# Optimization experiments

Hardware: AMD Instinct MI355X
Metric: run time of the kernel (lower is better)

Reference implementation:

```python
import jax, jax.numpy as jnp
import numpy as np

IN_FEATURES = 4096
OUT_FEATURES = 11008
BATCH = 16


def setup_inputs() -> dict:
    key = jax.random.key(0)
    k_x, k_w, k_s, k_b = jax.random.split(key, 4)
    x = jax.random.normal(k_x, (BATCH, IN_FEATURES), dtype=jnp.float32)
    # symmetric int8 weights stored as int32 for jax portability (values in [-127, 127])
    weight_int8 = jax.random.randint(k_w, (OUT_FEATURES, IN_FEATURES), -127, 128, dtype=jnp.int32)
    # per-output-channel scales, small positive values typical of int8 quantization
    weight_scale = jax.random.uniform(k_s, (OUT_FEATURES,), dtype=jnp.float32, minval=0.005, maxval=0.02)
    bias = jax.random.normal(k_b, (OUT_FEATURES,), dtype=jnp.float32)
    return {"x": x, "weight_int8": weight_int8, "weight_scale": weight_scale, "bias": bias}


def reference(x, weight_int8, weight_scale, bias):
    # Dequantize: w_dq[o, i] = int8[o, i] * scale[o]  -> fp32 [OUT, IN]
    w_dq = weight_int8.astype(x.dtype) * weight_scale[:, None]
    # F.linear: y = x @ w_dq.T + bias  -> [BATCH, OUT]
    return jnp.einsum("bi,oi->bo", x, w_dq) + bias
```

## Files before the change

kernel.cpp:

```cpp
#include <hip/hip_runtime.h>

#define IN_F   4096
#define OUT_F  11008
#define BATCH  16
#define TK     512
#define CO     16
#define BLOCK  256
#define SPLITK 4
#define KCHUNK (IN_F / SPLITK)

typedef int   i32x4 __attribute__((ext_vector_type(4)));

__global__ __launch_bounds__(BLOCK) void init_out_kernel(
    const float* __restrict__ bias, float* __restrict__ out)
{
    int idx = blockIdx.x * BLOCK + threadIdx.x;
    if (idx < BATCH * OUT_F) {
        int o = idx % OUT_F;
        out[idx] = bias[o];
    }
}

__global__ __launch_bounds__(BLOCK) void qlin_kernel(
    const float* __restrict__ x,
    const int*   __restrict__ w,
    const float* __restrict__ scale,
    float* __restrict__ out)
{
    __shared__ float xs[BATCH][TK];

    const int tid = threadIdx.x;
    const int tx  = tid & 63;
    const int ty  = tid >> 6;
    const int o0  = blockIdx.x * CO + ty * 4;
    const int kb  = blockIdx.y * KCHUNK;

    const i32x4* __restrict__ wbase = (const i32x4*)(w + (size_t)o0 * IN_F);

    float acc[64];
    #pragma unroll
    for (int i = 0; i < 64; ++i) acc[i] = 0.f;

    for (int k0 = kb; k0 < kb + KCHUNK; k0 += TK) {
        #pragma unroll
        for (int j = 0; j < (BATCH * TK / 4) / BLOCK; ++j) {
            int f  = tid + j * BLOCK;
            int b  = f >> 7;
            int kc = f & 127;
            const float* src = x + (size_t)b * IN_F + k0 + kc * 4;
            void* dst = (char*)&xs[0][0] + (size_t)f * 16;
            __builtin_amdgcn_global_load_lds(
                (const __attribute__((address_space(1))) void*)src,
                (__attribute__((address_space(3))) void*)dst,
                16, 0, 0);
        }
        __syncthreads();

        #pragma unroll
        for (int it = 0; it < TK / 256; ++it) {
            const int    kl  = it * 256 + tx * 4;
            const size_t kg4 = (size_t)((k0 >> 2) + it * 64 + tx);

            i32x4 w0 = __builtin_nontemporal_load(wbase + kg4);
            i32x4 w1 = __builtin_nontemporal_load(wbase + kg4 + 1 * (IN_F / 4));
            i32x4 w2 = __builtin_nontemporal_load(wbase + kg4 + 2 * (IN_F / 4));
            i32x4 w3 = __builtin_nontemporal_load(wbase + kg4 + 3 * (IN_F / 4));

            float wf[4][4];
            #pragma unroll
            for (int e = 0; e < 4; ++e) {
                wf[0][e] = (float)w0[e];
                wf[1][e] = (float)w1[e];
                wf[2][e] = (float)w2[e];
                wf[3][e] = (float)w3[e];
            }

            #pragma unroll
            for (int bc = 0; bc < 4; ++bc) {
                float4 xv[4];
                #pragma unroll
                for (int bb = 0; bb < 4; ++bb)
                    xv[bb] = *(const float4*)&xs[bc * 4 + bb][kl];

                #pragma unroll
                for (int r = 0; r < 4; ++r)
                    #pragma unroll
                    for (int bb = 0; bb < 4; ++bb) {
                        float a = acc[r * 16 + bc * 4 + bb];
                        a += wf[r][0] * xv[bb].x;
                        a += wf[r][1] * xv[bb].y;
                        a += wf[r][2] * xv[bb].z;
                        a += wf[r][3] * xv[bb].w;
                        acc[r * 16 + bc * 4 + bb] = a;
                    }
            }
        }
        __syncthreads();
    }

    #pragma unroll
    for (int wd = 32; wd >= 1; wd >>= 1) {
        const bool upper = (tx & wd) != 0;
        #pragma unroll
        for (int i = 0; i < wd; ++i) {
            float lo = acc[i]      + __shfl_xor(acc[i],      wd);
            float hi = acc[i + wd] + __shfl_xor(acc[i + wd], wd);
            acc[i] = upper ? hi : lo;
        }
    }

    const int o = o0 + (tx >> 4);
    const int b = tx & 15;
    atomicAdd(&out[(size_t)b * OUT_F + o], acc[0] * scale[o]);
}

extern "C" void kernel_launch(void* const* d_in, const int* in_sizes, int n_in,
                              void* d_out, int out_size, void* d_ws, size_t ws_size,
                              hipStream_t stream) {
    const float* x     = (const float*)d_in[0];
    const int*   w     = (const int*)d_in[1];
    const float* scale = (const float*)d_in[2];
    const float* bias  = (const float*)d_in[3];
    float* out = (float*)d_out;

    init_out_kernel<<<(BATCH * OUT_F + BLOCK - 1) / BLOCK, BLOCK, 0, stream>>>(bias, out);

    dim3 grid(OUT_F / CO, SPLITK);
    qlin_kernel<<<grid, dim3(BLOCK), 0, stream>>>(x, w, scale, out);
}
```

Measured before the change: 259.4 us.

## Stage full K chunk in LDS and prefetch all weight loads upfront

Replaces the tiled K loop with a single load of the block's entire K chunk of activations into shared memory. All weight vectors for the chunk are issued up front into registers before computing. This is meant to increase memory-level parallelism and remove intermediate barriers. In exchange it doubles LDS usage and raises register pressure, which can reduce occupancy.

```diff
diff --git a/kernel.cpp b/kernel.cpp
--- a/kernel.cpp
+++ b/kernel.cpp
@@ -3,11 +3,11 @@
 #define IN_F   4096
 #define OUT_F  11008
 #define BATCH  16
-#define TK     512
 #define CO     16
 #define BLOCK  256
 #define SPLITK 4
 #define KCHUNK (IN_F / SPLITK)
+#define NIT    (KCHUNK / 256)
 
 typedef int   i32x4 __attribute__((ext_vector_type(4)));
 
@@ -27,7 +27,7 @@
     const float* __restrict__ scale,
     float* __restrict__ out)
 {
-    __shared__ float xs[BATCH][TK];
+    __shared__ float xs[BATCH][KCHUNK];
 
     const int tid = threadIdx.x;
     const int tx  = tid & 63;
@@ -41,61 +41,59 @@
     #pragma unroll
     for (int i = 0; i < 64; ++i) acc[i] = 0.f;
 
-    for (int k0 = kb; k0 < kb + KCHUNK; k0 += TK) {
+    #pragma unroll
+    for (int j = 0; j < (BATCH * KCHUNK / 4) / BLOCK; ++j) {
+        int f  = tid + j * BLOCK;
+        int b  = f >> 8;
+        int kc = f & 255;
+        const float* src = x + (size_t)b * IN_F + kb + kc * 4;
+        void* dst = (char*)&xs[0][0] + (size_t)f * 16;
+        __builtin_amdgcn_global_load_lds(
+            (const __attribute__((address_space(1))) void*)src,
+            (__attribute__((address_space(3))) void*)dst,
+            16, 0, 0);
+    }
+    __syncthreads();
+
+    i32x4 wr[NIT][4];
+    #pragma unroll
+    for (int it = 0; it < NIT; ++it) {
+        const size_t kg4 = (size_t)((kb >> 2) + it * 64 + tx);
         #pragma unroll
-        for (int j = 0; j < (BATCH * TK / 4) / BLOCK; ++j) {
-            int f  = tid + j * BLOCK;
-            int b  = f >> 7;
-            int kc = f & 127;
-            const float* src = x + (size_t)b * IN_F + k0 + kc * 4;
-            void* dst = (char*)&xs[0][0] + (size_t)f * 16;
-            __builtin_amdgcn_global_load_lds(
-                (const __attribute__((address_space(1))) void*)src,
-                (__attribute__((address_space(3))) void*)dst,
-                16, 0, 0);
-        }
-        __syncthreads();
+        for (int r = 0; r < 4; ++r)
+            wr[it][r] = __builtin_nontemporal_load(wbase + kg4 + (size_t)r * (IN_F / 4));
+    }
+
+    #pragma unroll
+    for (int it = 0; it < NIT; ++it) {
+        const int kl = it * 256 + tx * 4;
+
+        float wf[4][4];
+        #pragma unroll
+        for (int r = 0; r < 4; ++r)
+            #pragma unroll
+            for (int e = 0; e < 4; ++e)
+                wf[r][e] = (float)wr[it][r][e];
 
         #pragma unroll
-        for (int it = 0; it < TK / 256; ++it) {
-            const int    kl  = it * 256 + tx * 4;
-            const size_t kg4 = (size_t)((k0 >> 2) + it * 64 + tx);
-
-            i32x4 w0 = __builtin_nontemporal_load(wbase + kg4);
-            i32x4 w1 = __builtin_nontemporal_load(wbase + kg4 + 1 * (IN_F / 4));
-            i32x4 w2 = __builtin_nontemporal_load(wbase + kg4 + 2 * (IN_F / 4));
-            i32x4 w3 = __builtin_nontemporal_load(wbase + kg4 + 3 * (IN_F / 4));
-
-            float wf[4][4];
+        for (int bc = 0; bc < 4; ++bc) {
+            float4 xv[4];
             #pragma unroll
-            for (int e = 0; e < 4; ++e) {
-                wf[0][e] = (float)w0[e];
-                wf[1][e] = (float)w1[e];
-                wf[2][e] = (float)w2[e];
-                wf[3][e] = (float)w3[e];
-            }
+            for (int bb = 0; bb < 4; ++bb)
+                xv[bb] = *(const float4*)&xs[bc * 4 + bb][kl];
 
             #pragma unroll
-            for (int bc = 0; bc < 4; ++bc) {
-                float4 xv[4];
+            for (int r = 0; r < 4; ++r)
                 #pragma unroll
-                for (int bb = 0; bb < 4; ++bb)
-                    xv[bb] = *(const float4*)&xs[bc * 4 + bb][kl];
-
-                #pragma unroll
-                for (int r = 0; r < 4; ++r)
-                    #pragma unroll
-                    for (int bb = 0; bb < 4; ++bb) {
-                        float a = acc[r * 16 + bc * 4 + bb];
-                        a += wf[r][0] * xv[bb].x;
-                        a += wf[r][1] * xv[bb].y;
-                        a += wf[r][2] * xv[bb].z;
-                        a += wf[r][3] * xv[bb].w;
-                        acc[r * 16 + bc * 4 + bb] = a;
-                    }
-            }
+                for (int bb = 0; bb < 4; ++bb) {
+                    float a = acc[r * 16 + bc * 4 + bb];
+                    a += wf[r][0] * xv[bb].x;
+                    a += wf[r][1] * xv[bb].y;
+                    a += wf[r][2] * xv[bb].z;
+                    a += wf[r][3] * xv[bb].w;
+                    acc[r * 16 + bc * 4 + bb] = a;
+                }
         }
-        __syncthreads();
     }
 
     #pragma unroll
```

Result: no change. 264.1 us (+1.8%).
